# Optimization experiments

Measured on AMD Instinct MI355X. Metric: run time of the kernel, lower is better.

The kernel has to match this reference:

```python
import jax, jax.numpy as jnp
import numpy as np

B, S, H, K = 64, 512, 1024, 7

def setup_inputs() -> dict:
    key = jax.random.key(0)
    ks = jax.random.split(key, 7)
    x = jax.random.normal(ks[0], (B, S, H), dtype=jnp.float32)
    gt = jax.random.randint(ks[1], (B, S), 0, K, dtype=jnp.int64)
    mask = jnp.ones((B, S), dtype=bool)
    # learned parameters
    W = jax.random.normal(ks[2], (H, K), dtype=jnp.float32) * (1.0 / np.sqrt(H))
    b = jnp.zeros((K,), dtype=jnp.float32)
    start_trans = jax.random.uniform(ks[3], (K,), minval=-0.1, maxval=0.1)
    end_trans = jax.random.uniform(ks[4], (K,), minval=-0.1, maxval=0.1)
    trans = jax.random.uniform(ks[5], (K, K), minval=-0.1, maxval=0.1)
    return {"x": x, "gt": gt, "mask": mask, "W": W, "b": b,
            "start_trans": start_trans, "end_trans": end_trans, "trans": trans}

def _crf_neg_llh(emissions, gt, mask, start_trans, end_trans, trans):
    # emissions: [B,S,K], gt: [B,S] int, mask: [B,S] bool
    maskf = mask.astype(emissions.dtype)
    # ---- numerator: score of gold path ----
    em_at_tag = jnp.take_along_axis(emissions, gt[..., None], axis=-1)[..., 0]  # [B,S]
    trans_sc = trans[gt[:, :-1], gt[:, 1:]]                                      # [B,S-1]
    num = start_trans[gt[:, 0]] + em_at_tag[:, 0]
    num = num + jnp.sum((trans_sc + em_at_tag[:, 1:]) * maskf[:, 1:], axis=1)
    last_idx = jnp.sum(mask, axis=1).astype(jnp.int32) - 1                       # [B]
    last_tags = jnp.take_along_axis(gt, last_idx[:, None], axis=1)[:, 0]
    num = num + end_trans[last_tags]
    # ---- denominator: log partition via forward algorithm (lax.scan) ----
    alpha0 = start_trans[None, :] + emissions[:, 0]                              # [B,K]
    em_rest = jnp.transpose(emissions[:, 1:], (1, 0, 2))                         # [S-1,B,K]
    m_rest = jnp.transpose(mask[:, 1:], (1, 0))                                  # [S-1,B]
    def step(alpha, inp):
        em_t, m_t = inp
        nxt = jax.nn.logsumexp(alpha[:, :, None] + trans[None, :, :] + em_t[:, None, :], axis=1)
        return jnp.where(m_t[:, None], nxt, alpha), None
    alpha, _ = jax.lax.scan(step, alpha0, (em_rest, m_rest))
    denom = jax.nn.logsumexp(alpha + end_trans[None, :], axis=1)                 # [B]
    llh = num - denom
    return -jnp.mean(llh)  # reduction='mean', module returns negative

def reference(x, gt, mask, W, b, start_trans, end_trans, trans):
    emissions = jnp.einsum('bsh,hk->bsk', x, W) + b
    return _crf_neg_llh(emissions, gt, mask, start_trans, end_trans, trans)
```

## Files before the change

kernel.cpp:

```cpp
#include <hip/hip_runtime.h>
#include <math.h>

#define NB 64
#define NS 512
#define NH 1024
#define NK 7
#define NCHUNK 16
#define CLEN 32

#define WS_CNT     0
#define WS_ALPHA0  80
#define WS_NUMP    (WS_ALPHA0 + 64 * 8)
#define WS_CHUNKP  (WS_NUMP + 64 * 16)
#define WS_LLH     (WS_CHUNKP + 64 * 16 * 49)

__global__ __launch_bounds__(512, 4) void crf_mega(
    const float* __restrict__ x, const float* __restrict__ W,
    const float* __restrict__ bias, const float* __restrict__ trans,
    const float* __restrict__ start_trans, const float* __restrict__ end_trans,
    const int* __restrict__ gt32,
    int* __restrict__ cnt, float* __restrict__ ws, float* __restrict__ out)
{
    __shared__ float4 lds_w4[14 * 128];
    __shared__ float lds_half[CLEN][2][8];
    __shared__ float lds_em[CLEN * 8];
    __shared__ float lds_tr[49];
    __shared__ float lds_C[NCHUNK * 49];

    float* __restrict__ alpha0g = ws + WS_ALPHA0;
    float* __restrict__ numP    = ws + WS_NUMP;
    float* __restrict__ chunkP  = ws + WS_CHUNKP;
    float* __restrict__ llh     = ws + WS_LLH;

    const int tid  = threadIdx.x;
    const int lane = tid & 63;
    const int wave = tid >> 6;
    const int pair = wave >> 1;
    const int half = wave & 1;
    const int b = blockIdx.x >> 4;
    const int c = blockIdx.x & (NCHUNK - 1);
    const int t0 = c * CLEN;
    const int row0 = b * NS + t0;

    if (tid < 49) lds_tr[tid] = trans[tid];

    {
        float* lds_wf = (float*)lds_w4;
#pragma unroll
        for (int q = 0; q < 14; ++q) {
            const int e = tid + 512 * q;
            const float val = W[e];
            const int h  = e / 7;
            const int k  = e - h * 7;
            const int hw = h >> 9;
            const int cw = (h >> 8) & 1;
            const int lw = (h >> 2) & 63;
            const int ii = h & 3;
            lds_wf[(((cw * 7 + k) * 2 + hw) * 64 + lw) * 4 + ii] = val;
        }
    }
    __syncthreads();

    float4 w4[2][NK];
#pragma unroll
    for (int cc = 0; cc < 2; ++cc)
#pragma unroll
        for (int k = 0; k < NK; ++k)
            w4[cc][k] = lds_w4[(cc * NK + k) * 128 + half * 64 + lane];

    const float4* xbase = (const float4*)(x + (size_t)row0 * NH) + half * 128 + lane;

#pragma unroll 2
    for (int s = 0; s < 8; ++s) {
        const int r = pair + 4 * s;
        const float4* xr = xbase + (size_t)r * (NH / 4);
        const float4 v0 = xr[0];
        const float4 v1 = xr[64];
        float acc[NK];
#pragma unroll
        for (int k = 0; k < NK; ++k)
            acc[k] = v0.x * w4[0][k].x + v0.y * w4[0][k].y
                   + v0.z * w4[0][k].z + v0.w * w4[0][k].w
                   + v1.x * w4[1][k].x + v1.y * w4[1][k].y
                   + v1.z * w4[1][k].z + v1.w * w4[1][k].w;
#pragma unroll
        for (int m = 1; m < 8; m <<= 1)
#pragma unroll
            for (int k = 0; k < NK; ++k)
                acc[k] += __shfl_xor(acc[k], m, 64);
        const int ss = lane & 7;
        const float v01 = (ss & 1) ? acc[1] : acc[0];
        const float v23 = (ss & 1) ? acc[3] : acc[2];
        const float v45 = (ss & 1) ? acc[5] : acc[4];
        const float w03 = (ss & 2) ? v23 : v01;
        const float w47 = (ss & 2) ? acc[6] : v45;
        float v = (ss & 4) ? w47 : w03;
        v += __shfl_xor(v, 8, 64);
        v += __shfl_xor(v, 16, 64);
        v += __shfl_xor(v, 32, 64);
        if (lane < NK) lds_half[r][half][lane] = v;
    }
    __syncthreads();

    if (tid < CLEN * NK) {
        const int r = tid / NK;
        const int k = tid - r * NK;
        lds_em[r * 8 + k] = lds_half[r][0][k] + lds_half[r][1][k] + bias[k];
    }
    __syncthreads();
    if (wave != 0) return;


    int oddbits = 0;
    for (int i = lane; i < 256; i += 64) oddbits |= gt32[2 * i + 1];
    const bool is64 = (__ballot(oddbits != 0) == 0ull);

    {
        const int tloc = lane & 31;
        const int tg = t0 + tloc;
        const int gidx = b * NS + tg;
        const int g = is64 ? gt32[2 * gidx] : gt32[gidx];
        float term = 0.f;
        if (lane < 32) {
            if (tg == 0) {
                term = start_trans[g] + lds_em[g];
            } else {
                const int pidx = gidx - 1;
                const int gp = is64 ? gt32[2 * pidx] : gt32[pidx];
                term = lds_tr[gp * 7 + g] + lds_em[tloc * 8 + g];
            }
            if (tg == NS - 1) term += end_trans[g];
        }
#pragma unroll
        for (int m = 1; m < 64; m <<= 1) term += __shfl_xor(term, m, 64);
        if (lane == 0) numP[b * NCHUNK + c] = term;
    }

    if (c == 0 && lane < NK)
        alpha0g[b * 8 + lane] = start_trans[lane] + lds_em[lane];

    {
        const int li = lane < 49 ? lane : 48;
        const int i = li / 7;
        const int k = li - i * 7;
        float tj[NK];
#pragma unroll
        for (int j = 0; j < NK; ++j) tj[j] = lds_tr[j * 7 + k];

        const int first = (c == 0) ? 1 : 0;
        float P = lds_tr[i * 7 + k] + lds_em[first * 8 + k];
        for (int t = first + 1; t < CLEN; ++t) {
            float a[NK];
#pragma unroll
            for (int j = 0; j < NK; ++j)
                a[j] = __shfl(P, i * 7 + j, 64) + tj[j];
            const float m = fmaxf(fmaxf(fmaxf(a[0], a[1]), fmaxf(a[2], a[3])),
                                  fmaxf(fmaxf(a[4], a[5]), a[6]));
            const float su = __expf(a[0]-m) + __expf(a[1]-m) + __expf(a[2]-m)
                           + __expf(a[3]-m) + __expf(a[4]-m) + __expf(a[5]-m)
                           + __expf(a[6]-m);
            P = m + __logf(su) + lds_em[t * 8 + k];
        }
        if (lane < 49)
            chunkP[(size_t)(b * NCHUNK + c) * 49 + lane] = P;
    }

    __threadfence();
    int old = 0;
    if (lane == 0) old = atomicAdd(&cnt[b], 1);
    old = __shfl(old, 0, 64);
    if (old != NCHUNK - 1) return;
    __threadfence();

    for (int idx = lane; idx < NCHUNK * 49; idx += 64)
        lds_C[idx] = chunkP[(size_t)b * NCHUNK * 49 + idx];

    float np = (lane < NCHUNK) ? numP[b * NCHUNK + lane] : 0.f;
#pragma unroll
    for (int m = 1; m < 16; m <<= 1) np += __shfl_xor(np, m, 64);
    const float num = __shfl(np, 0, 64);

    const int kk = lane < NK ? lane : NK - 1;
    float alpha = alpha0g[b * 8 + kk];
#pragma unroll
    for (int cc = 0; cc < NCHUNK; ++cc) {
        float a[NK];
#pragma unroll
        for (int j = 0; j < NK; ++j)
            a[j] = __shfl(alpha, j, 64) + lds_C[cc * 49 + j * 7 + kk];
        const float m = fmaxf(fmaxf(fmaxf(a[0], a[1]), fmaxf(a[2], a[3])),
                              fmaxf(fmaxf(a[4], a[5]), a[6]));
        const float su = __expf(a[0]-m) + __expf(a[1]-m) + __expf(a[2]-m)
                       + __expf(a[3]-m) + __expf(a[4]-m) + __expf(a[5]-m)
                       + __expf(a[6]-m);
        alpha = m + __logf(su);
    }

    float v = (lane < NK) ? (alpha + end_trans[kk]) : -3.0e38f;
    float mv = v;
#pragma unroll
    for (int m = 1; m < 8; m <<= 1) mv = fmaxf(mv, __shfl_xor(mv, m, 64));
    float e = (lane < NK) ? __expf(v - mv) : 0.f;
#pragma unroll
    for (int m = 1; m < 8; m <<= 1) e += __shfl_xor(e, m, 64);
    if (lane == 0) llh[b] = (mv + __logf(e)) - num;

    __threadfence();
    int old2 = 0;
    if (lane == 0) old2 = atomicAdd(&cnt[NB], 1);
    old2 = __shfl(old2, 0, 64);
    if (old2 != NB - 1) return;
    __threadfence();

    float s = llh[lane];
#pragma unroll
    for (int m = 1; m < 64; m <<= 1) s += __shfl_xor(s, m, 64);
    if (lane == 0) out[0] = s * (1.0f / NB);
}

extern "C" void kernel_launch(void* const* d_in, const int* in_sizes, int n_in,
                              void* d_out, int out_size, void* d_ws, size_t ws_size,
                              hipStream_t stream)
{
    const float* x    = (const float*)d_in[0];
    const int*   gt   = (const int*)d_in[1];
    const float* W    = (const float*)d_in[3];
    const float* bias = (const float*)d_in[4];
    const float* st   = (const float*)d_in[5];
    const float* et   = (const float*)d_in[6];
    const float* tr   = (const float*)d_in[7];

    int*   cnt = (int*)d_ws;
    float* ws  = (float*)d_ws;

    hipMemsetAsync(cnt, 0, 80 * sizeof(int), stream);
    crf_mega<<<NB * NCHUNK, 512, 0, stream>>>(x, W, bias, tr, st, et, gt,
                                              cnt, ws, (float*)d_out);
}
```

Before: 271.9 us.

## Hold full W slice in registers per lane and reduce with DPP/swizzle

```diff
diff --git a/kernel.cpp b/kernel.cpp
--- a/kernel.cpp
+++ b/kernel.cpp
@@ -14,15 +14,25 @@
 #define WS_CHUNKP  (WS_NUMP + 64 * 16)
 #define WS_LLH     (WS_CHUNKP + 64 * 16 * 49)
 
-__global__ __launch_bounds__(512, 4) void crf_mega(
+template <int CTRL>
+__device__ __forceinline__ float dpp_add(float v) {
+    const int sh = __builtin_amdgcn_update_dpp(0, __float_as_int(v),
+                                               CTRL, 0xF, 0xF, true);
+    return v + __int_as_float(sh);
+}
+template <int PAT>
+__device__ __forceinline__ float swz_add(float v) {
+    const int sh = __builtin_amdgcn_ds_swizzle(__float_as_int(v), PAT);
+    return v + __int_as_float(sh);
+}
+
+__global__ __launch_bounds__(256) void crf_mega(
     const float* __restrict__ x, const float* __restrict__ W,
     const float* __restrict__ bias, const float* __restrict__ trans,
     const float* __restrict__ start_trans, const float* __restrict__ end_trans,
     const int* __restrict__ gt32,
     int* __restrict__ cnt, float* __restrict__ ws, float* __restrict__ out)
 {
-    __shared__ float4 lds_w4[14 * 128];
-    __shared__ float lds_half[CLEN][2][8];
     __shared__ float lds_em[CLEN * 8];
     __shared__ float lds_tr[49];
     __shared__ float lds_C[NCHUNK * 49];
@@ -32,80 +42,57 @@
     float* __restrict__ chunkP  = ws + WS_CHUNKP;
     float* __restrict__ llh     = ws + WS_LLH;
 
-    const int tid  = threadIdx.x;
-    const int lane = tid & 63;
-    const int wave = tid >> 6;
-    const int pair = wave >> 1;
-    const int half = wave & 1;
+    const int lane = threadIdx.x & 63;
+    const int wave = threadIdx.x >> 6;
     const int b = blockIdx.x >> 4;
     const int c = blockIdx.x & (NCHUNK - 1);
     const int t0 = c * CLEN;
     const int row0 = b * NS + t0;
 
-    if (tid < 49) lds_tr[tid] = trans[tid];
-
-    {
-        float* lds_wf = (float*)lds_w4;
-#pragma unroll
-        for (int q = 0; q < 14; ++q) {
-            const int e = tid + 512 * q;
-            const float val = W[e];
-            const int h  = e / 7;
-            const int k  = e - h * 7;
-            const int hw = h >> 9;
-            const int cw = (h >> 8) & 1;
-            const int lw = (h >> 2) & 63;
-            const int ii = h & 3;
-            lds_wf[(((cw * 7 + k) * 2 + hw) * 64 + lw) * 4 + ii] = val;
-        }
-    }
-    __syncthreads();
-
-    float4 w4[2][NK];
-#pragma unroll
-    for (int cc = 0; cc < 2; ++cc)
-#pragma unroll
-        for (int k = 0; k < NK; ++k)
-            w4[cc][k] = lds_w4[(cc * NK + k) * 128 + half * 64 + lane];
-
-    const float4* xbase = (const float4*)(x + (size_t)row0 * NH) + half * 128 + lane;
-
-#pragma unroll 2
-    for (int s = 0; s < 8; ++s) {
-        const int r = pair + 4 * s;
-        const float4* xr = xbase + (size_t)r * (NH / 4);
-        const float4 v0 = xr[0];
-        const float4 v1 = xr[64];
+    if (threadIdx.x < 49) lds_tr[threadIdx.x] = trans[threadIdx.x];
+
+    float w[4][4][NK];
+#pragma unroll
+    for (int cc = 0; cc < 4; ++cc)
+#pragma unroll
+        for (int i = 0; i < 4; ++i) {
+            const int h = 4 * (cc * 64 + lane) + i;
+#pragma unroll
+            for (int k = 0; k < NK; ++k)
+                w[cc][i][k] = W[h * NK + k];
+        }
+    const float bl = bias[lane < NK ? lane : 0];
+
+    for (int r = wave; r < CLEN; r += 4) {
+        const float4* xr = (const float4*)(x + (size_t)(row0 + r) * NH);
         float acc[NK];
 #pragma unroll
-        for (int k = 0; k < NK; ++k)
-            acc[k] = v0.x * w4[0][k].x + v0.y * w4[0][k].y
-                   + v0.z * w4[0][k].z + v0.w * w4[0][k].w
-                   + v1.x * w4[1][k].x + v1.y * w4[1][k].y
-                   + v1.z * w4[1][k].z + v1.w * w4[1][k].w;
-#pragma unroll
-        for (int m = 1; m < 8; m <<= 1)
+        for (int k = 0; k < NK; ++k) acc[k] = 0.f;
+#pragma unroll
+        for (int cc = 0; cc < 4; ++cc) {
+            const float4 v = xr[cc * 64 + lane];
 #pragma unroll
             for (int k = 0; k < NK; ++k)
-                acc[k] += __shfl_xor(acc[k], m, 64);
-        const int ss = lane & 7;
-        const float v01 = (ss & 1) ? acc[1] : acc[0];
-        const float v23 = (ss & 1) ? acc[3] : acc[2];
-        const float v45 = (ss & 1) ? acc[5] : acc[4];
-        const float w03 = (ss & 2) ? v23 : v01;
-        const float w47 = (ss & 2) ? acc[6] : v45;
-        float v = (ss & 4) ? w47 : w03;
-        v += __shfl_xor(v, 8, 64);
-        v += __shfl_xor(v, 16, 64);
+                acc[k] += v.x * w[cc][0][k] + v.y * w[cc][1][k]
+                        + v.z * w[cc][2][k] + v.w * w[cc][3][k];
+        }
+#pragma unroll
+        for (int k = 0; k < NK; ++k) {
+            acc[k] = dpp_add<0xB1>(acc[k]);
+            acc[k] = dpp_add<0x4E>(acc[k]);
+            acc[k] = dpp_add<0x141>(acc[k]);
+        }
+        const int s = lane & 7;
+        const float v01 = (s & 1) ? acc[1] : acc[0];
+        const float v23 = (s & 1) ? acc[3] : acc[2];
+        const float v45 = (s & 1) ? acc[5] : acc[4];
+        const float w03 = (s & 2) ? v23 : v01;
+        const float w47 = (s & 2) ? acc[6] : v45;
+        float v = (s & 4) ? w47 : w03;
+        v = swz_add<0x201F>(v);
+        v = swz_add<0x401F>(v);
         v += __shfl_xor(v, 32, 64);
-        if (lane < NK) lds_half[r][half][lane] = v;
-    }
-    __syncthreads();
-
-    if (tid < CLEN * NK) {
-        const int r = tid / NK;
-        const int k = tid - r * NK;
-        lds_em[r * 8 + k] = lds_half[r][0][k] + lds_half[r][1][k] + bias[k];
+        if (lane < NK) lds_em[r * 8 + lane] = v + bl;
     }
     __syncthreads();
     if (wave != 0) return;
@@ -233,7 +220,7 @@
     int*   cnt = (int*)d_ws;
     float* ws  = (float*)d_ws;
 
-    hipMemsetAsync(cnt, 0, 80 * sizeof(int), stream);
-    crf_mega<<<NB * NCHUNK, 512, 0, stream>>>(x, W, bias, tr, st, et, gt,
+    (void)hipMemsetAsync(cnt, 0, 80 * sizeof(int), stream);
+    crf_mega<<<NB * NCHUNK, 256, 0, stream>>>(x, W, bias, tr, st, et, gt,
                                               cnt, ws, (float*)d_out);
 }
```

Result: no change. 271.2 us (-0.2%).
